# Kernel tuning notes

Measured on AMD Instinct MI355X. Metric: run time of the kernel, lower is better.

## Reference

```python
import jax, jax.numpy as jnp
import numpy as np

T, B, D = 64, 256, 2000
TN, E, H, A, V = 3000, 256, 256, 128, 128
PS, PE, S = 64, 64, 128
G1N, G1L, G2N, G2L = 1500, 4, 1500, 6


def setup_inputs():
    key = jax.random.key(0)
    ks = jax.random.split(key, 32)
    def nrm(k, shape, s=0.05):
        return jax.random.normal(k, shape, dtype=jnp.float32) * s
    inp = {}
    inp["X"] = jax.random.uniform(ks[0], (T, B, D), dtype=jnp.float32)
    inp["profiles"] = nrm(ks[1], (B, PS), 1.0)
    inp["ini_embd"] = nrm(ks[2], (TN, E), 1.0)
    inp["Wa_w"] = nrm(ks[3], (2 * E, A))
    inp["Wa_b"] = jnp.zeros((A,), jnp.float32)
    inp["Ua_w"] = nrm(ks[4], (A, 1))
    inp["gru_Wih"] = nrm(ks[5], (3 * H, E))
    inp["gru_Whh"] = nrm(ks[6], (3 * H, H))
    inp["gru_bih"] = jnp.zeros((3 * H,), jnp.float32)
    inp["gru_bhh"] = jnp.zeros((3 * H,), jnp.float32)
    inp["tranH_w"] = nrm(ks[7], (H + PE, E))
    inp["tranH_b"] = jnp.zeros((E,), jnp.float32)
    inp["out_w"] = nrm(ks[8], (H + V + PE, D))
    inp["out_b"] = jnp.zeros((D,), jnp.float32)
    inp["erase_w"] = nrm(ks[9], (E, V))
    inp["erase_b"] = jnp.zeros((V,), jnp.float32)
    inp["add_w"] = nrm(ks[10], (E, V))
    inp["add_b"] = jnp.zeros((V,), jnp.float32)
    inp["iniVam"] = nrm(ks[11], (S, V), 1.0)
    inp["emP_w"] = nrm(ks[12], (PS, PE))
    inp["emP_b"] = jnp.zeros((PE,), jnp.float32)
    inp["attnP_w"] = nrm(ks[13], (PE + V, PE))
    inp["attnP_b"] = jnp.zeros((PE,), jnp.float32)
    inp["KMIds"] = jax.random.randint(ks[14], (S,), 0, TN, dtype=jnp.int32)
    inp["leaves1"] = jax.random.randint(ks[15], (G1N, G1L), 0, TN, dtype=jnp.int32)
    inp["anc1"] = jax.random.randint(ks[16], (G1N, G1L), 0, TN, dtype=jnp.int32)
    inp["leaves2"] = jax.random.randint(ks[17], (G2N, G2L), 0, TN, dtype=jnp.int32)
    inp["anc2"] = jax.random.randint(ks[18], (G2N, G2L), 0, TN, dtype=jnp.int32)
    inp["mapInfo"] = jax.random.randint(ks[19], (D,), 0, G1N + G2N, dtype=jnp.int32)
    lens = jnp.sort(jax.random.randint(ks[20], (B,), 1, T + 1, dtype=jnp.int32))[::-1]
    inp["X_lengths"] = lens.at[0].set(T)
    return inp


def _forward(floats, ints):
    (X, profiles, ini_embd, Wa_w, Wa_b, Ua_w, gru_Wih, gru_Whh, gru_bih, gru_bhh,
     tranH_w, tranH_b, out_w, out_b, erase_w, erase_b, add_w, add_b, iniVam,
     emP_w, emP_b, attnP_w, attnP_b) = floats
    KMIds, leaves1, anc1, leaves2, anc2, mapInfo, X_lengths = ints

    # GRAM-style ontology attention over (leaf, ancestor) pairs, grouped by path length
    def group_embed(leaves, anc):
        le = ini_embd[leaves]                                     # [N,L,E]
        ae = ini_embd[anc]                                        # [N,L,E]
        hdn = jnp.tanh(jnp.concatenate([le, ae], axis=2) @ Wa_w + Wa_b)
        w = jax.nn.softmax(hdn @ Ua_w, axis=1)                    # [N,L,1]
        return jnp.sum(w * ae, axis=1)                            # [N,E]

    embedMat = jnp.concatenate([group_embed(leaves1, anc1),
                                group_embed(leaves2, anc2)], axis=0)[mapInfo]  # [D,E]
    Xe = jnp.einsum('tbd,de->tbe', X, embedMat)                   # [T,B,E]

    # packed-sequence GRU: frozen state / zero output beyond each sample's length
    mask = (jnp.arange(T)[:, None] < X_lengths[None, :])[..., None]  # [T,B,1]

    def gru_step(h, tup):
        x_t, m_t = tup
        gx = x_t @ gru_Wih.T + gru_bih
        gh = h @ gru_Whh.T + gru_bhh
        r = jax.nn.sigmoid(gx[:, :H] + gh[:, :H])
        z = jax.nn.sigmoid(gx[:, H:2 * H] + gh[:, H:2 * H])
        n = jnp.tanh(gx[:, 2 * H:] + r * gh[:, 2 * H:])
        h_new = (1.0 - z) * n + z * h
        h = jnp.where(m_t, h_new, h)
        return h, jnp.where(m_t, h, 0.0)

    h0 = jnp.zeros((B, H), jnp.float32)
    _, gru_out = jax.lax.scan(gru_step, h0, (Xe, mask))           # [T,B,H]

    prof = profiles @ emP_w + emP_b                               # [B,PE]
    prof_rep = jnp.broadcast_to(prof[None], (T, B, PE))
    tran = jnp.concatenate([gru_out, prof_rep], axis=2) @ tranH_w + tranH_b  # [T,B,E]
    KM = ini_embd[KMIds]                                          # [S,E]
    slot_w = jax.nn.softmax(jnp.einsum('tbe,se->tbs', tran, KM), axis=2)     # [T,B,S]

    # erase/add gates depend only on Xe -> precompute, then scan VM recurrence
    erase = jax.nn.sigmoid(Xe @ erase_w + erase_b)                # [T,B,V]
    add = jnp.tanh(Xe @ add_w + add_b)                            # [T,B,V]

    def mem_step(VM, tup):
        sw, er, ad = tup                                          # [B,S],[B,V],[B,V]
        read = jnp.einsum('bs,bsv->bv', sw, VM)
        VM = VM * (1.0 - sw[:, :, None] * er[:, None, :]) + sw[:, :, None] * ad[:, None, :]
        return VM, read

    VM0 = jnp.broadcast_to(iniVam[None], (B, S, V))
    _, read = jax.lax.scan(mem_step, VM0, (slot_w, erase, add))   # read: [T,B,V]

    attn = jax.nn.relu(jnp.concatenate([prof_rep, read], axis=2) @ attnP_w + attnP_b)
    prof2 = prof_rep * attn
    final = jnp.concatenate([gru_out, read, prof2], axis=2)       # [T,B,H+V+PE]
    # dropout is identity (eval / drop_rate=0)
    return jax.nn.softmax(final @ out_w + out_b, axis=2)          # [T,B,D]


def reference(X, profiles, ini_embd, Wa_w, Wa_b, Ua_w, gru_Wih, gru_Whh, gru_bih, gru_bhh, tranH_w, tranH_b, out_w, out_b, erase_w, erase_b, add_w, add_b, iniVam, emP_w, emP_b, attnP_w, attnP_b, KMIds, leaves1, anc1, leaves2, anc2, mapInfo, X_lengths):
    floats = (X, profiles, ini_embd, Wa_w, Wa_b, Ua_w, gru_Wih, gru_Whh, gru_bih, gru_bhh,
              tranH_w, tranH_b, out_w, out_b, erase_w, erase_b, add_w, add_b, iniVam,
              emP_w, emP_b, attnP_w, attnP_b)
    ints = (KMIds, leaves1, anc1, leaves2, anc2, mapInfo, X_lengths)
    return _forward(floats, ints)
```

## Files before the change

kernel.cpp:

```cpp
#include <hip/hip_runtime.h>
#include <hip/hip_bf16.h>
#include <cmath>

#define T_  64
#define B_  256
#define D_  2000
#define TN_ 3000
#define E_  256
#define H_  256
#define A_  128
#define V_  128
#define PS_ 64
#define PE_ 64
#define S_  128
#define G1N_ 1500
#define G1L_ 4
#define G2N_ 1500
#define G2L_ 6
#define M_  (T_ * B_)
#define KF_ (H_ + V_ + PE_)
#define NREG 28

typedef __attribute__((ext_vector_type(8))) short short8_t;
typedef __attribute__((ext_vector_type(4))) float floatx4;
typedef _Float16 __attribute__((ext_vector_type(2))) h2_t;
typedef _Float16 __attribute__((ext_vector_type(8))) h8_t;

static __device__ __forceinline__ float sigmoidf_(float x) {
    return 1.0f / (1.0f + __expf(-x));
}

static __device__ __forceinline__ void bsplit_(float v, __hip_bfloat16& hi, __hip_bfloat16& lo) {
    hi = __float2bfloat16(v);
    lo = __float2bfloat16(v - __bfloat162float(hi));
}

static __device__ __forceinline__ float dot2_(unsigned int w, unsigned int h, float acc) {
    union { unsigned int u; h2_t h; } cw, ch;
    cw.u = w; ch.u = h;
#if __has_builtin(__builtin_amdgcn_fdot2)
    return __builtin_amdgcn_fdot2(cw.h, ch.h, acc, false);
#else
    return acc + (float)cw.h[0] * (float)ch.h[0] + (float)cw.h[1] * (float)ch.h[1];
#endif
}

static __device__ __forceinline__ void gl_lds16(const void* g, void* l)
{
#if __has_builtin(__builtin_amdgcn_global_load_lds)
    __builtin_amdgcn_global_load_lds(
        (const __attribute__((address_space(1))) void*)g,
        (__attribute__((address_space(3))) void*)l, 16, 0, 0);
#else
    *(short8_t*)l = *(const short8_t*)g;
#endif
}

template<int DT>
static __device__ __forceinline__ floatx4 mfma16_(short8_t a, short8_t b, floatx4 c) {
    if constexpr (DT == 0) {
        return __builtin_amdgcn_mfma_f32_16x16x32_bf16(a, b, c, 0, 0, 0);
    } else {
        union { short8_t s; h8_t h; } ua, ub;
        ua.s = a; ub.s = b;
        return __builtin_amdgcn_mfma_f32_16x16x32_f16(ua.h, ub.h, c, 0, 0, 0);
    }
}

template<int EPI, bool ACCUM, int OUTMODE, int NPH, int DT>
__global__ __launch_bounds__(256)
void k_mgemm3(const __hip_bfloat16* __restrict__ Ahi, const __hip_bfloat16* __restrict__ Alo,
              const __hip_bfloat16* __restrict__ Bhi, const __hip_bfloat16* __restrict__ Blo,
              const float* __restrict__ bias, float* __restrict__ Cf,
              __hip_bfloat16* __restrict__ Chi, __hip_bfloat16* __restrict__ Clo,
              int K, int Nreal, int nblk)
{
    __shared__ __align__(16) short As[2][4096];
    __shared__ __align__(16) short Bs[2][4096];

    const int tid  = threadIdx.x;
    const int lane = tid & 63;
    const int w    = tid >> 6;
    const int wm   = w >> 1, wn = w & 1;
    const int lr   = lane & 15;
    const int lkc  = lane >> 4;

    const int bx = blockIdx.x;
    const int xcd = bx & 7, loc = bx >> 3;
    const int mchunk = (int)gridDim.x / (8 * nblk);
    const int m0 = (xcd * mchunk + loc / nblk) * 128;
    const int n0 = (loc % nblk) * 128;

    const int fa = 2 * w;
    const size_t aoff0 = (size_t)(m0 + fa * 16 + lr) * K + lkc * 8;
    const size_t aoff1 = aoff0 + (size_t)16 * K;
    const size_t boff0 = (size_t)(n0 + fa * 16 + lr) * K + lkc * 8;
    const size_t boff1 = boff0 + (size_t)16 * K;

    const int lA0 = (fa    ) * 512 + lane * 8;
    const int lA1 = (fa + 1) * 512 + lane * 8;

    floatx4 acc[4][4];
#pragma unroll
    for (int i = 0; i < 4; ++i)
#pragma unroll
        for (int j = 0; j < 4; ++j) acc[i][j] = floatx4{0.f, 0.f, 0.f, 0.f};

    const int KT = K >> 5;
    const int NT = NPH * KT;

    int s_ph = 0, s_k = 0;
    auto do_stage = [&](int buf) {
        const __hip_bfloat16* Ap = (s_ph == 2) ? Alo : Ahi;
        const __hip_bfloat16* Bp = (s_ph == 1) ? Blo : Bhi;
        gl_lds16(Ap + aoff0 + s_k, &As[buf][lA0]);
        gl_lds16(Ap + aoff1 + s_k, &As[buf][lA1]);
        gl_lds16(Bp + boff0 + s_k, &Bs[buf][lA0]);
        gl_lds16(Bp + boff1 + s_k, &Bs[buf][lA1]);
        s_k += 32;
        if (s_k >= K) { s_k = 0; ++s_ph; }
    };

    do_stage(0);
    __syncthreads();

#pragma unroll 1
    for (int t = 0; t < NT; ++t) {
        const int cur = t & 1;
        if (t + 1 < NT) do_stage(cur ^ 1);

        short8_t af[4], bf[4];
#pragma unroll
        for (int i = 0; i < 4; ++i)
            af[i] = *(const short8_t*)(const void*)&As[cur][(wm * 4 + i) * 512 + lane * 8];
#pragma unroll
        for (int j = 0; j < 4; ++j)
            bf[j] = *(const short8_t*)(const void*)&Bs[cur][(wn * 4 + j) * 512 + lane * 8];
#pragma unroll
        for (int i = 0; i < 4; ++i)
#pragma unroll
            for (int j = 0; j < 4; ++j)
                acc[i][j] = mfma16_<DT>(af[i], bf[j], acc[i][j]);

        __syncthreads();
    }

#pragma unroll
    for (int i = 0; i < 4; ++i) {
        const int row = m0 + wm * 64 + i * 16 + (lane >> 4) * 4;
#pragma unroll
        for (int j = 0; j < 4; ++j) {
            const int col = n0 + wn * 64 + j * 16 + (lane & 15);
            if (col < Nreal) {
                float bv = bias ? bias[col] : 0.0f;
#pragma unroll
                for (int r = 0; r < 4; ++r) {
                    float v = acc[i][j][r] + bv;
                    if (EPI == 1) v = (col < 128) ? sigmoidf_(v) : tanhf(v);
                    if (EPI == 2) {
                        if (col < 128) v = sigmoidf_(v);
                        else if (col < 256) v = tanhf(v);
                    }
                    size_t o = (size_t)(row + r) * Nreal + col;
                    if (OUTMODE == 0) {
                        if (ACCUM) v += Cf[o];
                        Cf[o] = v;
                    } else if (OUTMODE == 1) {
                        __hip_bfloat16 h, l;
                        bsplit_(v, h, l);
                        Chi[o] = h; Clo[o] = l;
                    } else {
                        ((_Float16*)Chi)[o] = (_Float16)v;
                    }
                }
            }
        }
    }
}

__global__ __launch_bounds__(256)
void k_cvtX(const float* __restrict__ X, _Float16* __restrict__ XH)
{
    int idx = blockIdx.x * blockDim.x + threadIdx.x;
    if (idx >= M_ * 256) return;
    int m = idx >> 8, d0 = (idx & 255) * 8;
    _Float16 h[8];
    if (d0 + 7 < D_) {
        float4 p = *(const float4*)(X + (size_t)m * D_ + d0);
        float4 q = *(const float4*)(X + (size_t)m * D_ + d0 + 4);
        h[0]=(_Float16)p.x; h[1]=(_Float16)p.y; h[2]=(_Float16)p.z; h[3]=(_Float16)p.w;
        h[4]=(_Float16)q.x; h[5]=(_Float16)q.y; h[6]=(_Float16)q.z; h[7]=(_Float16)q.w;
    } else {
#pragma unroll
        for (int i = 0; i < 8; ++i)
            h[i] = (d0 + i < D_) ? (_Float16)X[(size_t)m * D_ + d0 + i] : (_Float16)0.0f;
    }
    *(short8_t*)(XH + (size_t)m * 2048 + d0) = *(short8_t*)h;
}

__global__ __launch_bounds__(256)
void k_mgemmXh(const _Float16* __restrict__ XH,
               const _Float16* __restrict__ Bhi, const _Float16* __restrict__ Blo,
               __hip_bfloat16* __restrict__ Chi, __hip_bfloat16* __restrict__ Clo)
{
    const int KP = 2048, NN = 256, nblk = 2;
    __shared__ __align__(16) short Ah[2][4096];
    __shared__ __align__(16) short Bh[2][4096];
    __shared__ __align__(16) short Bl[2][4096];

    const int tid  = threadIdx.x;
    const int lane = tid & 63;
    const int w    = tid >> 6;
    const int wm   = w >> 1, wn = w & 1;
    const int lr   = lane & 15;
    const int lkc  = lane >> 4;

    const int bx = blockIdx.x;
    const int xcd = bx & 7, loc = bx >> 3;
    const int mchunk = 256 / (8 * nblk);
    const int m0 = (xcd * mchunk + loc / nblk) * 128;
    const int n0 = (loc % nblk) * 128;

    const int fa = 2 * w;
    const size_t aoff0 = (size_t)(m0 + fa * 16 + lr) * KP + lkc * 8;
    const size_t aoff1 = aoff0 + (size_t)16 * KP;
    const size_t boff0 = (size_t)(n0 + fa * 16 + lr) * KP + lkc * 8;
    const size_t boff1 = boff0 + (size_t)16 * KP;

    const int lA0 = (fa    ) * 512 + lane * 8;
    const int lA1 = (fa + 1) * 512 + lane * 8;

    floatx4 acc[4][4];
#pragma unroll
    for (int i = 0; i < 4; ++i)
#pragma unroll
        for (int j = 0; j < 4; ++j) acc[i][j] = floatx4{0.f, 0.f, 0.f, 0.f};

    int s_k = 0;
    auto do_stage = [&](int buf) {
        gl_lds16(XH  + aoff0 + s_k, &Ah[buf][lA0]);
        gl_lds16(XH  + aoff1 + s_k, &Ah[buf][lA1]);
        gl_lds16(Bhi + boff0 + s_k, &Bh[buf][lA0]);
        gl_lds16(Bhi + boff1 + s_k, &Bh[buf][lA1]);
        gl_lds16(Blo + boff0 + s_k, &Bl[buf][lA0]);
        gl_lds16(Blo + boff1 + s_k, &Bl[buf][lA1]);
        s_k += 32;
    };

    do_stage(0);
    __syncthreads();

#pragma unroll 1
    for (int t = 0; t < KP / 32; ++t) {
        const int cur = t & 1;
        if (s_k < KP) do_stage(cur ^ 1);

        short8_t af[4], bfh[4], bfl[4];
#pragma unroll
        for (int i = 0; i < 4; ++i) {
            af[i]  = *(const short8_t*)(const void*)&Ah[cur][(wm * 4 + i) * 512 + lane * 8];
            bfh[i] = *(const short8_t*)(const void*)&Bh[cur][(wn * 4 + i) * 512 + lane * 8];
        }
#pragma unroll
        for (int i = 0; i < 4; ++i)
#pragma unroll
            for (int j = 0; j < 4; ++j)
                acc[i][j] = mfma16_<1>(af[i], bfh[j], acc[i][j]);
#pragma unroll
        for (int j = 0; j < 4; ++j)
            bfl[j] = *(const short8_t*)(const void*)&Bl[cur][(wn * 4 + j) * 512 + lane * 8];
#pragma unroll
        for (int i = 0; i < 4; ++i)
#pragma unroll
            for (int j = 0; j < 4; ++j)
                acc[i][j] = mfma16_<1>(af[i], bfl[j], acc[i][j]);

        __syncthreads();
    }

#pragma unroll
    for (int i = 0; i < 4; ++i) {
        const int row = m0 + wm * 64 + i * 16 + (lane >> 4) * 4;
#pragma unroll
        for (int j = 0; j < 4; ++j) {
            const int col = n0 + wn * 64 + j * 16 + (lane & 15);
#pragma unroll
            for (int r = 0; r < 4; ++r) {
                float v = acc[i][j][r];
                size_t o = (size_t)(row + r) * NN + col;
                __hip_bfloat16 h, l;
                bsplit_(v, h, l);
                Chi[o] = h; Clo[o] = l;
            }
        }
    }
}

template<int BM, int BN, int BK, int TM, int TN>
__global__ __launch_bounds__(256)
void k_gemm(const float* __restrict__ A, const float* __restrict__ B,
            float* __restrict__ C, int M, int N, int K)
{
    __shared__ float As[BK][BM + 4];
    __shared__ float Bs[BK][BN + 4];
    const int tid = threadIdx.y * blockDim.x + threadIdx.x;
    const int m0 = blockIdx.y * BM;
    const int n0 = blockIdx.x * BN;
    float acc[TM][TN];
#pragma unroll
    for (int i = 0; i < TM; ++i)
#pragma unroll
        for (int j = 0; j < TN; ++j) acc[i][j] = 0.0f;
    for (int k0 = 0; k0 < K; k0 += BK) {
#pragma unroll
        for (int i = tid; i < BM * BK; i += 256) {
            int r = i / BK, c = i % BK;
            int m = m0 + r;
            As[c][r] = (m < M) ? A[(size_t)m * K + k0 + c] : 0.0f;
        }
#pragma unroll
        for (int i = tid; i < BK * BN; i += 256) {
            int r = i / BN, c = i % BN;
            Bs[r][c] = B[(size_t)(k0 + r) * N + n0 + c];
        }
        __syncthreads();
#pragma unroll
        for (int kk = 0; kk < BK; ++kk) {
            float a[TM], b[TN];
#pragma unroll
            for (int i = 0; i < TM; ++i) a[i] = As[kk][threadIdx.y * TM + i];
#pragma unroll
            for (int j = 0; j < TN; ++j) b[j] = Bs[kk][threadIdx.x * TN + j];
#pragma unroll
            for (int i = 0; i < TM; ++i)
#pragma unroll
                for (int j = 0; j < TN; ++j) acc[i][j] += a[i] * b[j];
        }
        __syncthreads();
    }
#pragma unroll
    for (int i = 0; i < TM; ++i) {
        int m = m0 + threadIdx.y * TM + i;
        if (m >= M) continue;
#pragma unroll
        for (int j = 0; j < TN; ++j)
            C[(size_t)m * N + n0 + threadIdx.x * TN + j] = acc[i][j];
    }
}

__global__ void k_pack_w2(const float* __restrict__ Wa_w, float* __restrict__ W2)
{
    int idx = blockIdx.x * blockDim.x + threadIdx.x;
    if (idx >= E_ * 2 * A_) return;
    int e = idx / (2 * A_), j = idx % (2 * A_);
    W2[idx] = (j < A_) ? Wa_w[(size_t)e * A_ + j]
                       : Wa_w[(size_t)(E_ + e) * A_ + (j - A_)];
}

__global__ void k_wg_split(const float* __restrict__ erase_w, const float* __restrict__ add_w,
                           const float* __restrict__ Wih,
                           const float* __restrict__ erase_b, const float* __restrict__ add_b,
                           const float* __restrict__ bih,
                           __hip_bfloat16* __restrict__ WGhi, __hip_bfloat16* __restrict__ WGlo,
                           float* __restrict__ biasG)
{
    int idx = blockIdx.x * blockDim.x + threadIdx.x;
    if (idx < 1024 * 256) {
        int n = idx >> 8, k = idx & 255;
        float v;
        if (n < 128)      v = erase_w[(size_t)k * V_ + n];
        else if (n < 256) v = add_w[(size_t)k * V_ + (n - 128)];
        else              v = Wih[(size_t)(n - 256) * 256 + k];
        bsplit_(v, WGhi[idx], WGlo[idx]);
    }
    if (idx < 1024)
        biasG[idx] = (idx < 128) ? erase_b[idx]
                   : (idx < 256) ? add_b[idx - 128]
                                 : bih[idx - 256];
}

__global__ void k_tranHT_split(const float* __restrict__ tranH_w,
                               __hip_bfloat16* __restrict__ hi, __hip_bfloat16* __restrict__ lo)
{
    int idx = blockIdx.x * blockDim.x + threadIdx.x;
    if (idx >= 256 * 320) return;
    int n = idx / 320, k = idx % 320;
    bsplit_(tranH_w[(size_t)k * 256 + n], hi[idx], lo[idx]);
}

__global__ void k_outWT_f16(const float* __restrict__ out_w, _Float16* __restrict__ dst)
{
    int idx = blockIdx.x * blockDim.x + threadIdx.x;
    if (idx >= 2048 * 448) return;
    int n = idx / 448, k = idx % 448;
    float v = (n < D_) ? out_w[(size_t)k * D_ + n] : 0.0f;
    dst[idx] = (_Float16)v;
}

__global__ void k_km_split(const float* __restrict__ ini_embd, const int* __restrict__ KMIds,
                           __hip_bfloat16* __restrict__ hi, __hip_bfloat16* __restrict__ lo)
{
    int idx = blockIdx.x * blockDim.x + threadIdx.x;
    if (idx >= S_ * E_) return;
    int s = idx / E_, k = idx % E_;
    bsplit_(ini_embd[(size_t)KMIds[s] * E_ + k], hi[idx], lo[idx]);
}

__global__ void k_embMT_f16(const float* __restrict__ embG, const int* __restrict__ mapInfo,
                            _Float16* __restrict__ hi, _Float16* __restrict__ lo)
{
    int idx = blockIdx.x * blockDim.x + threadIdx.x;
    if (idx >= 256 * 2048) return;
    int e = idx >> 11, d = idx & 2047;
    float v = (d < D_) ? embG[(size_t)mapInfo[d] * E_ + e] : 0.0f;
    _Float16 h = (_Float16)v;
    hi[idx] = h;
    lo[idx] = (_Float16)(v - (float)h);
}

__global__ void k_wgru_pack(const float* __restrict__ Whh,
                            unsigned int* __restrict__ Wrg, unsigned int* __restrict__ Wst)
{
    int idx = blockIdx.x * blockDim.x + threadIdx.x;
    if (idx >= 768 * 128) return;
    int j = idx / 128, e2 = idx % 128;
    union { unsigned int u; h2_t h; } c;
    c.h[0] = (_Float16)Whh[(size_t)j * 256 + 2 * e2];
    c.h[1] = (_Float16)Whh[(size_t)j * 256 + 2 * e2 + 1];
    if (e2 < 4 * NREG) {
        Wrg[(size_t)e2 * 768 + j] = c.u;
    } else {
        int ee = e2 - 4 * NREG;
        Wst[((size_t)(ee >> 2) * 768 + j) * 4 + (ee & 3)] = c.u;
    }
}

__global__ void k_prof(const float* __restrict__ profiles, const float* __restrict__ emP_w,
                       const float* __restrict__ emP_b, float* __restrict__ prof)
{
    int b = blockIdx.x, j = threadIdx.x;
    float acc = emP_b[j];
    for (int k = 0; k < PS_; ++k) acc += profiles[(size_t)b * PS_ + k] * emP_w[(size_t)k * PE_ + j];
    prof[(size_t)b * PE_ + j] = acc;
}

__global__ void k_fill_tp(const float* __restrict__ prof,
                          __hip_bfloat16* __restrict__ At_hi, __hip_bfloat16* __restrict__ At_lo)
{
    int idx = blockIdx.x * blockDim.x + threadIdx.x;
    if (idx >= M_ * PE_) return;
    int m = idx >> 6, pe = idx & 63;
    float v = prof[(size_t)(m & (B_ - 1)) * PE_ + pe];
    size_t o = (size_t)m * 320 + 256 + pe;
    bsplit_(v, At_hi[o], At_lo[o]);
}

__global__ void k_group_embed(const float* __restrict__ PP, const float* __restrict__ Wa_b,
                              const float* __restrict__ Ua_w, const float* __restrict__ ini_embd,
                              const int* __restrict__ leaves1, const int* __restrict__ anc1,
                              const int* __restrict__ leaves2, const int* __restrict__ anc2,
                              float* __restrict__ embedG)
{
    int n = blockIdx.x;
    int lane = threadIdx.x;
    const int* lv; const int* ac; int L;
    if (n < G1N_) { L = G1L_; lv = leaves1 + (size_t)n * G1L_; ac = anc1 + (size_t)n * G1L_; }
    else { int n2 = n - G1N_; L = G2L_; lv = leaves2 + (size_t)n2 * G2L_; ac = anc2 + (size_t)n2 * G2L_; }

    float score[6]; int ai[6];
    for (int l = 0; l < L; ++l) {
        int li = lv[l]; int av = ac[l]; ai[l] = av;
        float s = 0.0f;
        for (int a = lane; a < A_; a += 64) {
            float hv = tanhf(PP[(size_t)li * 256 + a] + PP[(size_t)av * 256 + 128 + a] + Wa_b[a]);
            s += hv * Ua_w[a];
        }
        for (int o = 32; o; o >>= 1) s += __shfl_xor(s, o);
        score[l] = s;
    }
    float mx = -1e30f;
    for (int l = 0; l < L; ++l) mx = fmaxf(mx, score[l]);
    float w[6], sum = 0.0f;
    for (int l = 0; l < L; ++l) { w[l] = __expf(score[l] - mx); sum += w[l]; }
    float inv = 1.0f / sum;
    for (int e = lane; e < E_; e += 64) {
        float acc = 0.0f;
        for (int l = 0; l < L; ++l) acc += w[l] * inv * ini_embd[(size_t)ai[l] * E_ + e];
        embedG[(size_t)n * E_ + e] = acc;
    }
}

__global__ __launch_bounds__(768, 3)
void k_gru5(const float* __restrict__ Cg, const unsigned int* __restrict__ Wrg,
            const uint4* __restrict__ Wst, const float* __restrict__ bhh,
            const int* __restrict__ X_len, float* __restrict__ gruo,
            __hip_bfloat16* __restrict__ At_hi, __hip_bfloat16* __restrict__ At_lo)
{
    const int b = blockIdx.x;
    const int tid = threadIdx.x;

    __shared__ uint4 h2S[32];
    __shared__ float ghS[768];
    __shared__ float gxnS[256];

    if (tid < 128) ((unsigned int*)h2S)[tid] = 0u;

    uint4 Wr[NREG];
#pragma unroll
    for (int c = 0; c < NREG; ++c) {
        Wr[c].x = Wrg[(size_t)(4 * c + 0) * 768 + tid];
        Wr[c].y = Wrg[(size_t)(4 * c + 1) * 768 + tid];
        Wr[c].z = Wrg[(size_t)(4 * c + 2) * 768 + tid];
        Wr[c].w = Wrg[(size_t)(4 * c + 3) * 768 + tid];
    }

    float hreg = 0.0f;
    const int len = X_len[b];
    const float bj = bhh[tid];
    __syncthreads();

    for (int t = 0; t < T_; ++t) {
        float gxv = Cg[((size_t)t * B_ + b) * 1024 + 256 + tid];

        float a0 = bj;
#pragma unroll
        for (int c = 0; c < 32; ++c) {
            uint4 w = (c < NREG) ? Wr[c] : Wst[(size_t)(c - NREG) * 768 + tid];
            uint4 h = h2S[c];
            a0 = dot2_(w.x, h.x, a0);
            a0 = dot2_(w.y, h.y, a0);
            a0 = dot2_(w.z, h.z, a0);
            a0 = dot2_(w.w, h.w, a0);
        }

        if (tid < 512) ghS[tid] = a0 + gxv;
        else { ghS[tid] = a0; gxnS[tid - 512] = gxv; }
        __syncthreads();

        if (tid < 256) {
            float r  = sigmoidf_(ghS[tid]);
            float z  = sigmoidf_(ghS[256 + tid]);
            float nn = tanhf(gxnS[tid] + r * ghS[512 + tid]);
            float hnew = (1.0f - z) * nn + z * hreg;
            bool msk = (t < len);
            hreg = msk ? hnew : hreg;
            float ov = msk ? hreg : 0.0f;
            size_t m = (size_t)t * B_ + b;
            gruo[m * H_ + tid] = ov;
            size_t o = m * 320 + tid;
            bsplit_(ov, At_hi[o], At_lo[o]);
            float partner = __shfl_xor(hreg, 1);
            if (!(tid & 1)) {
                union { unsigned int u; h2_t h; } p;
                p.h[0] = (_Float16)hreg;
                p.h[1] = (_Float16)partner;
                ((unsigned int*)h2S)[tid >> 1] = p.u;
            }
        }
        __syncthreads();
    }
}

__global__ __launch_bounds__(256)
void k_mem(const float* __restrict__ slotw, const float* __restrict__ Cg,
           const float* __restrict__ iniVam, float* __restrict__ readv)
{
    const int b = blockIdx.x;
    const int tid = threadIdx.x;
    const int v = tid & (V_ - 1);
    const int sh = tid >> 7;
    const int sbase = sh * 64;

    float VM[64];
#pragma unroll
    for (int i = 0; i < 64; ++i) VM[i] = iniVam[(size_t)(sbase + i) * V_ + v];

    __shared__ float swL[S_];
    __shared__ float eaL[2 * V_];
    __shared__ float part[V_];

    for (int t = 0; t < T_; ++t) {
        size_t m = (size_t)t * B_ + b;
        if (tid < S_) swL[tid] = slotw[m * S_ + tid];
        eaL[tid] = Cg[m * 1024 + tid];
        __syncthreads();

        float er = eaL[v], ad = eaL[V_ + v];
        float p0 = 0.0f, p1 = 0.0f, p2 = 0.0f, p3 = 0.0f;
#pragma unroll
        for (int i = 0; i < 16; ++i) {
            float s0 = swL[sbase + 4 * i];
            float s1 = swL[sbase + 4 * i + 1];
            float s2 = swL[sbase + 4 * i + 2];
            float s3 = swL[sbase + 4 * i + 3];
            float v0 = VM[4 * i], v1 = VM[4 * i + 1], v2 = VM[4 * i + 2], v3 = VM[4 * i + 3];
            p0 += s0 * v0; p1 += s1 * v1; p2 += s2 * v2; p3 += s3 * v3;
            VM[4 * i]     = v0 * (1.0f - s0 * er) + s0 * ad;
            VM[4 * i + 1] = v1 * (1.0f - s1 * er) + s1 * ad;
            VM[4 * i + 2] = v2 * (1.0f - s2 * er) + s2 * ad;
            VM[4 * i + 3] = v3 * (1.0f - s3 * er) + s3 * ad;
        }
        float acc = (p0 + p1) + (p2 + p3);
        if (sh == 1) part[v] = acc;
        __syncthreads();
        if (sh == 0) readv[m * V_ + v] = acc + part[v];
        __syncthreads();
    }
}

__global__ __launch_bounds__(256)
void k_build_final(const float* __restrict__ gruo, const float* __restrict__ readv,
                   const float* __restrict__ prof, const float* __restrict__ attnP_w,
                   const float* __restrict__ attnP_b, _Float16* __restrict__ F)
{
    const int m = blockIdx.x;
    const int b = m & (B_ - 1);
    const int tid = threadIdx.x;
    __shared__ float rd[V_];
    __shared__ float pf[PE_];
    if (tid < V_) rd[tid] = readv[(size_t)m * V_ + tid];
    if (tid < PE_) pf[tid] = prof[(size_t)b * PE_ + tid];
    __syncthreads();

    size_t base = (size_t)m * KF_;
    F[base + tid] = (_Float16)gruo[(size_t)m * H_ + tid];
    if (tid < V_) F[base + H_ + tid] = (_Float16)rd[tid];
    if (tid < PE_) {
        float a = attnP_b[tid];
        for (int k = 0; k < PE_; ++k) a += pf[k] * attnP_w[(size_t)k * PE_ + tid];
        for (int k = 0; k < V_; ++k) a += rd[k] * attnP_w[(size_t)(PE_ + k) * PE_ + tid];
        a = fmaxf(a, 0.0f);
        F[base + H_ + V_ + tid] = (_Float16)(pf[tid] * a);
    }
}

__global__ void k_softmax128(float* __restrict__ C)
{
    const int m = blockIdx.x;
    const size_t base = (size_t)m * S_;
    const int lane = threadIdx.x;
    float a = C[base + lane], b = C[base + 64 + lane];
    float mx = fmaxf(a, b);
    for (int o = 32; o; o >>= 1) mx = fmaxf(mx, __shfl_xor(mx, o));
    float e0 = __expf(a - mx), e1 = __expf(b - mx);
    float s = e0 + e1;
    for (int o = 32; o; o >>= 1) s += __shfl_xor(s, o);
    float inv = 1.0f / s;
    C[base + lane] = e0 * inv;
    C[base + 64 + lane] = e1 * inv;
}

__global__ __launch_bounds__(256)
void k_softmax2000(const _Float16* __restrict__ L, float* __restrict__ C)
{
    const int m = blockIdx.x;
    const size_t base = (size_t)m * D_;
    const int tid = threadIdx.x;
    const int wid = tid >> 6, lane = tid & 63;
    __shared__ float red[4], red2[4];

    float v[8];
#pragma unroll
    for (int i = 0; i < 8; ++i) {
        int d = i * 256 + tid;
        v[i] = (d < D_) ? (float)L[base + d] : -1e30f;
    }
    float mx = v[0];
#pragma unroll
    for (int i = 1; i < 8; ++i) mx = fmaxf(mx, v[i]);
    for (int o = 32; o; o >>= 1) mx = fmaxf(mx, __shfl_xor(mx, o));
    if (lane == 0) red[wid] = mx;
    __syncthreads();
    mx = fmaxf(fmaxf(red[0], red[1]), fmaxf(red[2], red[3]));

    float sum = 0.0f;
#pragma unroll
    for (int i = 0; i < 8; ++i) { v[i] = __expf(v[i] - mx); sum += v[i]; }
    for (int o = 32; o; o >>= 1) sum += __shfl_xor(sum, o);
    if (lane == 0) red2[wid] = sum;
    __syncthreads();
    sum = red2[0] + red2[1] + red2[2] + red2[3];
    float inv = 1.0f / sum;
#pragma unroll
    for (int i = 0; i < 8; ++i) {
        int d = i * 256 + tid;
        if (d < D_) C[base + d] = v[i] * inv;
    }
}

extern "C" void kernel_launch(void* const* d_in, const int* in_sizes, int n_in,
                              void* d_out, int out_size, void* d_ws, size_t ws_size,
                              hipStream_t stream)
{
    const float* X        = (const float*)d_in[0];
    const float* profiles = (const float*)d_in[1];
    const float* ini_embd = (const float*)d_in[2];
    const float* Wa_w     = (const float*)d_in[3];
    const float* Wa_b     = (const float*)d_in[4];
    const float* Ua_w     = (const float*)d_in[5];
    const float* gru_Wih  = (const float*)d_in[6];
    const float* gru_Whh  = (const float*)d_in[7];
    const float* gru_bih  = (const float*)d_in[8];
    const float* gru_bhh  = (const float*)d_in[9];
    const float* tranH_w  = (const float*)d_in[10];
    const float* tranH_b  = (const float*)d_in[11];
    const float* out_w    = (const float*)d_in[12];
    const float* out_b    = (const float*)d_in[13];
    const float* erase_w  = (const float*)d_in[14];
    const float* erase_b  = (const float*)d_in[15];
    const float* add_w    = (const float*)d_in[16];
    const float* add_b    = (const float*)d_in[17];
    const float* iniVam   = (const float*)d_in[18];
    const float* emP_w    = (const float*)d_in[19];
    const float* emP_b    = (const float*)d_in[20];
    const float* attnP_w  = (const float*)d_in[21];
    const float* attnP_b  = (const float*)d_in[22];
    const int* KMIds   = (const int*)d_in[23];
    const int* leaves1 = (const int*)d_in[24];
    const int* anc1    = (const int*)d_in[25];
    const int* leaves2 = (const int*)d_in[26];
    const int* anc2    = (const int*)d_in[27];
    const int* mapInfo = (const int*)d_in[28];
    const int* X_len   = (const int*)d_in[29];

    char* ws = (char*)d_ws;
    float* out = (float*)d_out;
    typedef __hip_bfloat16 bf16;

    const size_t R0 = 0;
    const size_t R1 = 67108864;
    const size_t R2 = 83886080;
    const size_t R3 = 100663296;
    size_t P = 121634816;
    const size_t EMBHI = P; P += 1048576;
    const size_t EMBLO = P; P += 1048576;
    const size_t OWF  = P; P += 1835008;
    const size_t WGHI = P; P += 524288;
    const size_t WGLO = P; P += 524288;
    const size_t THHI = P; P += 163840;
    const size_t THLO = P; P += 163840;
    const size_t KMHI = P; P += 65536;
    const size_t KMLO = P; P += 65536;
    const size_t WRG  = P; P += 344064;
    const size_t WST  = P; P += 49152;
    const size_t PROF = P; P += 65536;
    const size_t BIAS = P; P += 4096;
    const size_t W2O  = P; P += 262144;

    float* PP      = (float*)(ws + R0);
    float* embG    = (float*)(ws + R0 + 12288000);
    _Float16* XH   = (_Float16*)(ws + R0);
    float* Cg      = (float*)(ws + R0);
    _Float16* F16  = (_Float16*)(ws + R0);
    _Float16* LG16 = (_Float16*)(ws + 16777216);
    float* gruo    = (float*)(ws + R1);
    bf16*  Xe_hi   = (bf16*)(ws + R2);
    bf16*  Xe_lo   = (bf16*)(ws + R2 + 8388608);
    bf16*  tran_hi = (bf16*)(ws + R2);
    bf16*  tran_lo = (bf16*)(ws + R2 + 8388608);
    bf16*  At_hi   = (bf16*)(ws + R3);
    bf16*  At_lo   = (bf16*)(ws + R3 + 10485760);
    float* slotw   = (float*)(ws + R3);
    float* readv   = (float*)(ws + R3 + 10485760);
    _Float16* EMBhi = (_Float16*)(ws + EMBHI);
    _Float16* EMBlo = (_Float16*)(ws + EMBLO);
    _Float16* OWf = (_Float16*)(ws + OWF);
    bf16*  WGhi = (bf16*)(ws + WGHI); bf16* WGlo = (bf16*)(ws + WGLO);
    bf16*  THhi = (bf16*)(ws + THHI); bf16* THlo = (bf16*)(ws + THLO);
    bf16*  KMhi = (bf16*)(ws + KMHI); bf16* KMlo = (bf16*)(ws + KMLO);
    unsigned int* Wrg = (unsigned int*)(ws + WRG);
    unsigned int* Wst = (unsigned int*)(ws + WST);
    float* prof  = (float*)(ws + PROF);
    float* biasG = (float*)(ws + BIAS);
    float* W2p   = (float*)(ws + W2O);

    k_pack_w2<<<(E_ * 2 * A_ + 255) / 256, 256, 0, stream>>>(Wa_w, W2p);
    k_wg_split<<<(1024 * 256 + 255) / 256, 256, 0, stream>>>(
        erase_w, add_w, gru_Wih, erase_b, add_b, gru_bih, WGhi, WGlo, biasG);
    k_tranHT_split<<<(256 * 320 + 255) / 256, 256, 0, stream>>>(tranH_w, THhi, THlo);
    k_outWT_f16<<<(2048 * 448 + 255) / 256, 256, 0, stream>>>(out_w, OWf);
    k_km_split<<<(S_ * E_ + 255) / 256, 256, 0, stream>>>(ini_embd, KMIds, KMhi, KMlo);
    k_wgru_pack<<<(768 * 128 + 255) / 256, 256, 0, stream>>>(gru_Whh, Wrg, Wst);
    k_prof<<<B_, PE_, 0, stream>>>(profiles, emP_w, emP_b, prof);

    {
        dim3 blk(16, 16);
        dim3 grid(4, (TN_ + 63) / 64);
        k_gemm<64, 64, 16, 4, 4><<<grid, blk, 0, stream>>>(ini_embd, W2p, PP, TN_, 256, E_);
    }
    k_group_embed<<<G1N_ + G2N_, 64, 0, stream>>>(PP, Wa_b, Ua_w, ini_embd,
                                                  leaves1, anc1, leaves2, anc2, embG);
    k_embMT_f16<<<(256 * 2048) / 256, 256, 0, stream>>>(embG, mapInfo, EMBhi, EMBlo);

    k_cvtX<<<(M_ * 256) / 256, 256, 0, stream>>>(X, XH);

    k_mgemmXh<<<128 * 2, 256, 0, stream>>>(XH, EMBhi, EMBlo, Xe_hi, Xe_lo);

    k_mgemm3<2, false, 0, 3, 0><<<128 * 8, 256, 0, stream>>>(Xe_hi, Xe_lo, WGhi, WGlo,
        biasG, Cg, nullptr, nullptr, 256, 1024, 8);

    k_gru5<<<256, 768, 0, stream>>>(Cg, Wrg, (const uint4*)Wst, gru_bhh, X_len,
                                    gruo, At_hi, At_lo);
    k_fill_tp<<<(M_ * PE_) / 256, 256, 0, stream>>>(prof, At_hi, At_lo);

    k_mgemm3<0, false, 1, 3, 0><<<128 * 2, 256, 0, stream>>>(At_hi, At_lo, THhi, THlo,
        tranH_b, nullptr, tran_hi, tran_lo, 320, 256, 2);

    k_mgemm3<0, false, 0, 3, 0><<<128 * 1, 256, 0, stream>>>(tran_hi, tran_lo, KMhi, KMlo,
        nullptr, slotw, nullptr, nullptr, 256, 128, 1);

    k_softmax128<<<M_, 64, 0, stream>>>(slotw);
    k_mem<<<B_, 256, 0, stream>>>(slotw, Cg, iniVam, readv);
    k_build_final<<<M_, 256, 0, stream>>>(gruo, readv, prof, attnP_w, attnP_b, F16);

    k_mgemm3<0, false, 2, 1, 1><<<128 * 16, 256, 0, stream>>>(
        (const bf16*)F16, nullptr, (const bf16*)OWf, nullptr,
        out_b, nullptr, (bf16*)LG16, nullptr, 448, 2000, 16);

    k_softmax2000<<<M_, 256, 0, stream>>>(LG16, out);
}
```

Measured before the change: 671.6 us.

## Merge weight-packing kernels, fold profile fill into GRU, rebalance GRU weight registers

```diff
diff --git a/kernel.cpp b/kernel.cpp
--- a/kernel.cpp
+++ b/kernel.cpp
@@ -19,7 +19,7 @@
 #define G2L_ 6
 #define M_  (T_ * B_)
 #define KF_ (H_ + V_ + PE_)
-#define NREG 28
+#define NREG 24
 
 typedef __attribute__((ext_vector_type(8))) short short8_t;
 typedef __attribute__((ext_vector_type(4))) float floatx4;
@@ -348,62 +348,88 @@
     }
 }
 
-__global__ void k_pack_w2(const float* __restrict__ Wa_w, float* __restrict__ W2)
+__global__ __launch_bounds__(256)
+void k_packall(const float* __restrict__ Wa_w,
+               const float* __restrict__ erase_w, const float* __restrict__ add_w,
+               const float* __restrict__ Wih,
+               const float* __restrict__ erase_b, const float* __restrict__ add_b,
+               const float* __restrict__ bih,
+               const float* __restrict__ tranH_w, const float* __restrict__ out_w,
+               const float* __restrict__ ini_embd, const int* __restrict__ KMIds,
+               const float* __restrict__ Whh,
+               float* __restrict__ W2p,
+               __hip_bfloat16* __restrict__ WGhi, __hip_bfloat16* __restrict__ WGlo,
+               float* __restrict__ biasG,
+               __hip_bfloat16* __restrict__ THhi, __hip_bfloat16* __restrict__ THlo,
+               _Float16* __restrict__ OWf,
+               __hip_bfloat16* __restrict__ KMhi, __hip_bfloat16* __restrict__ KMlo,
+               unsigned int* __restrict__ Wrg, unsigned int* __restrict__ Wst)
 {
     int idx = blockIdx.x * blockDim.x + threadIdx.x;
-    if (idx >= E_ * 2 * A_) return;
-    int e = idx / (2 * A_), j = idx % (2 * A_);
-    W2[idx] = (j < A_) ? Wa_w[(size_t)e * A_ + j]
-                       : Wa_w[(size_t)(E_ + e) * A_ + (j - A_)];
-}
-
-__global__ void k_wg_split(const float* __restrict__ erase_w, const float* __restrict__ add_w,
-                           const float* __restrict__ Wih,
-                           const float* __restrict__ erase_b, const float* __restrict__ add_b,
-                           const float* __restrict__ bih,
-                           __hip_bfloat16* __restrict__ WGhi, __hip_bfloat16* __restrict__ WGlo,
-                           float* __restrict__ biasG)
-{
-    int idx = blockIdx.x * blockDim.x + threadIdx.x;
-    if (idx < 1024 * 256) {
+    if (idx < 65536) {
+        int e = idx >> 8, j = idx & 255;
+        W2p[idx] = (j < A_) ? Wa_w[(size_t)e * A_ + j]
+                            : Wa_w[(size_t)(E_ + e) * A_ + (j - A_)];
+        return;
+    }
+    idx -= 65536;
+    if (idx < 262144) {
         int n = idx >> 8, k = idx & 255;
         float v;
         if (n < 128)      v = erase_w[(size_t)k * V_ + n];
         else if (n < 256) v = add_w[(size_t)k * V_ + (n - 128)];
         else              v = Wih[(size_t)(n - 256) * 256 + k];
         bsplit_(v, WGhi[idx], WGlo[idx]);
-    }
-    if (idx < 1024)
+        return;
+    }
+    idx -= 262144;
+    if (idx < 1024) {
         biasG[idx] = (idx < 128) ? erase_b[idx]
                    : (idx < 256) ? add_b[idx - 128]
                                  : bih[idx - 256];
-}
-
-__global__ void k_tranHT_split(const float* __restrict__ tranH_w,
-                               __hip_bfloat16* __restrict__ hi, __hip_bfloat16* __restrict__ lo)
-{
-    int idx = blockIdx.x * blockDim.x + threadIdx.x;
-    if (idx >= 256 * 320) return;
-    int n = idx / 320, k = idx % 320;
-    bsplit_(tranH_w[(size_t)k * 256 + n], hi[idx], lo[idx]);
-}
-
-__global__ void k_outWT_f16(const float* __restrict__ out_w, _Float16* __restrict__ dst)
-{
-    int idx = blockIdx.x * blockDim.x + threadIdx.x;
-    if (idx >= 2048 * 448) return;
-    int n = idx / 448, k = idx % 448;
-    float v = (n < D_) ? out_w[(size_t)k * D_ + n] : 0.0f;
-    dst[idx] = (_Float16)v;
-}
-
-__global__ void k_km_split(const float* __restrict__ ini_embd, const int* __restrict__ KMIds,
-                           __hip_bfloat16* __restrict__ hi, __hip_bfloat16* __restrict__ lo)
-{
-    int idx = blockIdx.x * blockDim.x + threadIdx.x;
-    if (idx >= S_ * E_) return;
-    int s = idx / E_, k = idx % E_;
-    bsplit_(ini_embd[(size_t)KMIds[s] * E_ + k], hi[idx], lo[idx]);
+        return;
+    }
+    idx -= 1024;
+    if (idx < 81920) {
+        int n = idx / 320, k = idx % 320;
+        bsplit_(tranH_w[(size_t)k * 256 + n], THhi[idx], THlo[idx]);
+        return;
+    }
+    idx -= 81920;
+    if (idx < 917504) {
+        int n = idx / 448, k = idx % 448;
+        OWf[idx] = (n < D_) ? (_Float16)out_w[(size_t)k * D_ + n] : (_Float16)0.0f;
+        return;
+    }
+    idx -= 917504;
+    if (idx < 32768) {
+        int s = idx >> 8, k = idx & 255;
+        bsplit_(ini_embd[(size_t)KMIds[s] * E_ + k], KMhi[idx], KMlo[idx]);
+        return;
+    }
+    idx -= 32768;
+    if (idx < 98304) {
+        int j = idx / 128, e2 = idx % 128;
+        union { unsigned int u; h2_t h; } c;
+        c.h[0] = (_Float16)Whh[(size_t)j * 256 + 2 * e2];
+        c.h[1] = (_Float16)Whh[(size_t)j * 256 + 2 * e2 + 1];
+        if (e2 < 4 * NREG) {
+            int ch = e2 >> 2, i = e2 & 3;
+            Wrg[((size_t)ch * 768 + j) * 4 + i] = c.u;
+        } else {
+            int ee = e2 - 4 * NREG;
+            Wst[((size_t)(ee >> 2) * 768 + j) * 4 + (ee & 3)] = c.u;
+        }
+    }
+}
+
+__global__ void k_prof(const float* __restrict__ profiles, const float* __restrict__ emP_w,
+                       const float* __restrict__ emP_b, float* __restrict__ prof)
+{
+    int b = blockIdx.x, j = threadIdx.x;
+    float acc = emP_b[j];
+    for (int k = 0; k < PS_; ++k) acc += profiles[(size_t)b * PS_ + k] * emP_w[(size_t)k * PE_ + j];
+    prof[(size_t)b * PE_ + j] = acc;
 }
 
 __global__ void k_embMT_f16(const float* __restrict__ embG, const int* __restrict__ mapInfo,
@@ -416,43 +442,6 @@
     _Float16 h = (_Float16)v;
     hi[idx] = h;
     lo[idx] = (_Float16)(v - (float)h);
-}
-
-__global__ void k_wgru_pack(const float* __restrict__ Whh,
-                            unsigned int* __restrict__ Wrg, unsigned int* __restrict__ Wst)
-{
-    int idx = blockIdx.x * blockDim.x + threadIdx.x;
-    if (idx >= 768 * 128) return;
-    int j = idx / 128, e2 = idx % 128;
-    union { unsigned int u; h2_t h; } c;
-    c.h[0] = (_Float16)Whh[(size_t)j * 256 + 2 * e2];
-    c.h[1] = (_Float16)Whh[(size_t)j * 256 + 2 * e2 + 1];
-    if (e2 < 4 * NREG) {
-        Wrg[(size_t)e2 * 768 + j] = c.u;
-    } else {
-        int ee = e2 - 4 * NREG;
-        Wst[((size_t)(ee >> 2) * 768 + j) * 4 + (ee & 3)] = c.u;
-    }
-}
-
-__global__ void k_prof(const float* __restrict__ profiles, const float* __restrict__ emP_w,
-                       const float* __restrict__ emP_b, float* __restrict__ prof)
-{
-    int b = blockIdx.x, j = threadIdx.x;
-    float acc = emP_b[j];
-    for (int k = 0; k < PS_; ++k) acc += profiles[(size_t)b * PS_ + k] * emP_w[(size_t)k * PE_ + j];
-    prof[(size_t)b * PE_ + j] = acc;
-}
-
-__global__ void k_fill_tp(const float* __restrict__ prof,
-                          __hip_bfloat16* __restrict__ At_hi, __hip_bfloat16* __restrict__ At_lo)
-{
-    int idx = blockIdx.x * blockDim.x + threadIdx.x;
-    if (idx >= M_ * PE_) return;
-    int m = idx >> 6, pe = idx & 63;
-    float v = prof[(size_t)(m & (B_ - 1)) * PE_ + pe];
-    size_t o = (size_t)m * 320 + 256 + pe;
-    bsplit_(v, At_hi[o], At_lo[o]);
 }
 
 __global__ void k_group_embed(const float* __restrict__ PP, const float* __restrict__ Wa_b,
@@ -491,9 +480,10 @@
 }
 
 __global__ __launch_bounds__(768, 3)
-void k_gru5(const float* __restrict__ Cg, const unsigned int* __restrict__ Wrg,
-            const uint4* __restrict__ Wst, const float* __restrict__ bhh,
-            const int* __restrict__ X_len, float* __restrict__ gruo,
+void k_gru6(const float* __restrict__ Cg, const uint4* __restrict__ Wrg4,
+            const uint4* __restrict__ Wst4, const float* __restrict__ bhh,
+            const int* __restrict__ X_len, const float* __restrict__ prof,
+            float* __restrict__ gruo,
             __hip_bfloat16* __restrict__ At_hi, __hip_bfloat16* __restrict__ At_lo)
 {
     const int b = blockIdx.x;
@@ -508,29 +498,44 @@
     uint4 Wr[NREG];
 #pragma unroll
     for (int c = 0; c < NREG; ++c) {
-        Wr[c].x = Wrg[(size_t)(4 * c + 0) * 768 + tid];
-        Wr[c].y = Wrg[(size_t)(4 * c + 1) * 768 + tid];
-        Wr[c].z = Wrg[(size_t)(4 * c + 2) * 768 + tid];
-        Wr[c].w = Wrg[(size_t)(4 * c + 3) * 768 + tid];
+        Wr[c] = Wrg4[(size_t)c * 768 + tid];
+        asm volatile("" : "+v"(Wr[c].x), "+v"(Wr[c].y), "+v"(Wr[c].z), "+v"(Wr[c].w));
     }
 
     float hreg = 0.0f;
     const int len = X_len[b];
     const float bj = bhh[tid];
+
+    __hip_bfloat16 phi, plo;
+    if (tid >= 256 && tid < 320)
+        bsplit_(prof[(size_t)b * PE_ + (tid - 256)], phi, plo);
+
     __syncthreads();
 
     for (int t = 0; t < T_; ++t) {
         float gxv = Cg[((size_t)t * B_ + b) * 1024 + 256 + tid];
 
+        uint4 Wsv[8];
+#pragma unroll
+        for (int s = 0; s < 8; ++s)
+            Wsv[s] = Wst4[(size_t)s * 768 + tid];
+
         float a0 = bj;
 #pragma unroll
-        for (int c = 0; c < 32; ++c) {
-            uint4 w = (c < NREG) ? Wr[c] : Wst[(size_t)(c - NREG) * 768 + tid];
+        for (int c = 0; c < NREG; ++c) {
             uint4 h = h2S[c];
-            a0 = dot2_(w.x, h.x, a0);
-            a0 = dot2_(w.y, h.y, a0);
-            a0 = dot2_(w.z, h.z, a0);
-            a0 = dot2_(w.w, h.w, a0);
+            a0 = dot2_(Wr[c].x, h.x, a0);
+            a0 = dot2_(Wr[c].y, h.y, a0);
+            a0 = dot2_(Wr[c].z, h.z, a0);
+            a0 = dot2_(Wr[c].w, h.w, a0);
+        }
+#pragma unroll
+        for (int s = 0; s < 8; ++s) {
+            uint4 h = h2S[NREG + s];
+            a0 = dot2_(Wsv[s].x, h.x, a0);
+            a0 = dot2_(Wsv[s].y, h.y, a0);
+            a0 = dot2_(Wsv[s].z, h.z, a0);
+            a0 = dot2_(Wsv[s].w, h.w, a0);
         }
 
         if (tid < 512) ghS[tid] = a0 + gxv;
@@ -556,6 +561,10 @@
                 p.h[1] = (_Float16)partner;
                 ((unsigned int*)h2S)[tid >> 1] = p.u;
             }
+        } else if (tid < 320) {
+            size_t o = ((size_t)t * B_ + b) * 320 + tid;
+            At_hi[o] = phi;
+            At_lo[o] = plo;
         }
         __syncthreads();
     }
@@ -741,8 +750,8 @@
     const size_t THLO = P; P += 163840;
     const size_t KMHI = P; P += 65536;
     const size_t KMLO = P; P += 65536;
-    const size_t WRG  = P; P += 344064;
-    const size_t WST  = P; P += 49152;
+    const size_t WRG  = P; P += 294912;
+    const size_t WST  = P; P += 98304;
     const size_t PROF = P; P += 65536;
     const size_t BIAS = P; P += 4096;
     const size_t W2O  = P; P += 262144;
@@ -774,13 +783,9 @@
     float* biasG = (float*)(ws + BIAS);
     float* W2p   = (float*)(ws + W2O);
 
-    k_pack_w2<<<(E_ * 2 * A_ + 255) / 256, 256, 0, stream>>>(Wa_w, W2p);
-    k_wg_split<<<(1024 * 256 + 255) / 256, 256, 0, stream>>>(
-        erase_w, add_w, gru_Wih, erase_b, add_b, gru_bih, WGhi, WGlo, biasG);
-    k_tranHT_split<<<(256 * 320 + 255) / 256, 256, 0, stream>>>(tranH_w, THhi, THlo);
-    k_outWT_f16<<<(2048 * 448 + 255) / 256, 256, 0, stream>>>(out_w, OWf);
-    k_km_split<<<(S_ * E_ + 255) / 256, 256, 0, stream>>>(ini_embd, KMIds, KMhi, KMlo);
-    k_wgru_pack<<<(768 * 128 + 255) / 256, 256, 0, stream>>>(gru_Whh, Wrg, Wst);
+    k_packall<<<5700, 256, 0, stream>>>(Wa_w, erase_w, add_w, gru_Wih,
+        erase_b, add_b, gru_bih, tranH_w, out_w, ini_embd, KMIds, gru_Whh,
+        W2p, WGhi, WGlo, biasG, THhi, THlo, OWf, KMhi, KMlo, Wrg, Wst);
     k_prof<<<B_, PE_, 0, stream>>>(profiles, emP_w, emP_b, prof);
 
     {
@@ -799,9 +804,8 @@
     k_mgemm3<2, false, 0, 3, 0><<<128 * 8, 256, 0, stream>>>(Xe_hi, Xe_lo, WGhi, WGlo,
         biasG, Cg, nullptr, nullptr, 256, 1024, 8);
 
-    k_gru5<<<256, 768, 0, stream>>>(Cg, Wrg, (const uint4*)Wst, gru_bhh, X_len,
-                                    gruo, At_hi, At_lo);
-    k_fill_tp<<<(M_ * PE_) / 256, 256, 0, stream>>>(prof, At_hi, At_lo);
+    k_gru6<<<256, 768, 0, stream>>>(Cg, (const uint4*)Wrg, (const uint4*)Wst,
+                                    gru_bhh, X_len, prof, gruo, At_hi, At_lo);
 
     k_mgemm3<0, false, 1, 3, 0><<<128 * 2, 256, 0, stream>>>(At_hi, At_lo, THhi, THlo,
         tranH_b, nullptr, tran_hi, tran_lo, 320, 256, 2);
```

New measurement: 673.9 us. No clear change (+0.4%).
